# Optimization experiments

Hardware: AMD Instinct MI355X
Metric: run time of the kernel (lower is better)

The kernel has to match this reference:

```python
import jax, jax.numpy as jnp
import numpy as np

N, E, IN, H, OUT, G = 40000, 640000, 128, 128, 16, 64


def _sage(x, src, dst, Wl, Wr, b, n):
    # PyG SAGEConv (aggr='mean'): out = lin_l(mean_j x_j) + lin_r(x_i); bias in lin_l only
    msg = jnp.take(x, src, axis=0)                      # [E, d] gather
    s = jax.ops.segment_sum(msg, dst, num_segments=n)   # [N, d] scatter-add
    cnt = jax.ops.segment_sum(jnp.ones((src.shape[0], 1), x.dtype), dst, num_segments=n)
    agg = s / jnp.maximum(cnt, 1.0)                     # mean; 0 for isolated nodes
    return agg @ Wl.T + x @ Wr.T + b


def setup_inputs() -> dict:
    key = jax.random.key(0)
    ks = jax.random.split(key, 12)
    x = jax.random.normal(ks[0], (N, IN), jnp.float32)
    edge_index = jax.random.randint(ks[1], (2, E), 0, N, jnp.int64)
    batch = jnp.sort(jax.random.randint(ks[2], (N,), 0, G, jnp.int64))
    def lin(k, o, i):
        return jax.random.normal(k, (o, i), jnp.float32) / np.sqrt(i)
    return {
        "x": x, "edge_index": edge_index, "batch": batch,
        "W1l": lin(ks[3], H, IN), "W1r": lin(ks[4], H, IN), "b1": jnp.zeros((H,), jnp.float32),
        "W2l": lin(ks[5], H, H),  "W2r": lin(ks[6], H, H),  "b2": jnp.zeros((H,), jnp.float32),
        "W3l": lin(ks[7], H, H),  "W3r": lin(ks[8], H, H),  "b3": jnp.zeros((H,), jnp.float32),
        "Wfc": lin(ks[9], OUT, H), "bfc": jnp.zeros((OUT,), jnp.float32),
    }


def reference(x, edge_index, batch, W1l, W1r, b1, W2l, W2r, b2, W3l, W3r, b3, Wfc, bfc):
    src, dst = edge_index[0], edge_index[1]
    n = x.shape[0]
    h = jax.nn.relu(_sage(x, src, dst, W1l, W1r, b1, n))
    h = jax.nn.relu(_sage(h, src, dst, W2l, W2r, b2, n))
    h = jax.nn.relu(_sage(h, src, dst, W3l, W3r, b3, n))
    # global_mean_pool over graph ids
    s = jax.ops.segment_sum(h, batch, num_segments=G)
    cnt = jax.ops.segment_sum(jnp.ones((n, 1), h.dtype), batch, num_segments=G)
    pooled = s / jnp.maximum(cnt, 1.0)                  # [G, H]
    return pooled @ Wfc.T + bfc                          # [G, OUT]
```

## Files before the change

### kernel.cpp

```cpp
#include <hip/hip_runtime.h>

static constexpr int D = 128;
static constexpr int PS = 32;

typedef __attribute__((ext_vector_type(8))) short short8;
typedef __attribute__((ext_vector_type(4))) float f32x4;

__device__ inline ushort f2bf(float f) {
  union { float f; unsigned u; } v; v.f = f;
  unsigned r = v.u + 0x7FFF + ((v.u >> 16) & 1);
  return (ushort)(r >> 16);
}
__device__ inline float bf2f_lo(unsigned p) {
  union { unsigned u; float f; } v; v.u = p << 16; return v.f;
}
__device__ inline float bf2f_hi(unsigned p) {
  union { unsigned u; float f; } v; v.u = p & 0xFFFF0000u; return v.f;
}

__global__ __launch_bounds__(256) void k_hist(const int* __restrict__ dst, int* __restrict__ hist, int E) {
  int e = blockIdx.x * 256 + threadIdx.x;
  if (e < E) atomicAdd(&hist[dst[e]], 1);
}

__global__ __launch_bounds__(1024) void k_scan(const int* __restrict__ hist, int* __restrict__ offsets, int n) {
  __shared__ int wsum[16];
  int tid = threadIdx.x, lane = tid & 63, w = tid >> 6;
  int carry = 0;
  for (int base = 0; base < n; base += 1024) {
    int i = base + tid;
    int v = (i < n) ? hist[i] : 0;
    int x = v;
    #pragma unroll
    for (int off = 1; off < 64; off <<= 1) {
      int t = __shfl_up(x, off);
      if (lane >= off) x += t;
    }
    if (lane == 63) wsum[w] = x;
    __syncthreads();
    int wpre = 0, total = 0;
    #pragma unroll
    for (int k = 0; k < 16; ++k) { int s = wsum[k]; total += s; if (k < w) wpre += s; }
    if (i < n) offsets[i] = carry + wpre + x - v;
    carry += total;
    __syncthreads();
  }
  if (tid == 0) offsets[n] = carry;
}

__global__ __launch_bounds__(256) void k_fill(const int* __restrict__ src, const int* __restrict__ dst,
                                              const int* __restrict__ offsets, int* __restrict__ cursor,
                                              int* __restrict__ ssrc, int E) {
  int e = blockIdx.x * 256 + threadIdx.x;
  if (e < E) {
    int d = dst[e];
    int pos = offsets[d] + atomicAdd(&cursor[d], 1);
    ssrc[pos] = src[e];
  }
}

__global__ __launch_bounds__(256) void k_cvt(const float* __restrict__ in, ushort* __restrict__ out, int n4) {
  int i = blockIdx.x * 256 + threadIdx.x;
  if (i >= n4) return;
  float4 v = *(const float4*)&in[i * 4];
  ushort4 o;
  o.x = f2bf(v.x); o.y = f2bf(v.y); o.z = f2bf(v.z); o.w = f2bf(v.w);
  *(ushort4*)&out[i * 4] = o;
}

struct WPtrs { const float* s[6]; ushort* d[6]; };
__global__ __launch_bounds__(256) void k_cvt_w(WPtrs p) {
  int idx = blockIdx.x * 256 + threadIdx.x;
  int mat = idx >> 12;
  int off = (idx & 4095) * 4;
  float4 v = *(const float4*)&p.s[mat][off];
  ushort4 o;
  o.x = f2bf(v.x); o.y = f2bf(v.y); o.z = f2bf(v.z); o.w = f2bf(v.w);
  *(ushort4*)&p.d[mat][off] = o;
}

__global__ __launch_bounds__(256) void k_aggregate_bf(const ushort* __restrict__ X, const int* __restrict__ offsets,
                                                      const int* __restrict__ ssrc, ushort* __restrict__ Agg, int n) {
  int wid = (blockIdx.x * 256 + threadIdx.x) >> 6;
  int lane = threadIdx.x & 63;
  if (wid >= n) return;
  int q = lane >> 4, r = lane & 15;
  int o0 = offsets[wid], o1 = offsets[wid + 1];
  int deg = o1 - o0;

  float acc[8];
  #pragma unroll
  for (int i = 0; i < 8; ++i) acc[i] = 0.f;

  uint4 cur = {0u, 0u, 0u, 0u};
  if (q < deg) {
    int sid = ssrc[o0 + q];
    cur = *(const uint4*)&X[(size_t)sid * D + r * 8];
  }
  for (int base = 0; base < deg; base += 4) {
    uint4 nxt = {0u, 0u, 0u, 0u};
    int nb = base + 4 + q;
    if (nb < deg) {
      int sid = ssrc[o0 + nb];
      nxt = *(const uint4*)&X[(size_t)sid * D + r * 8];
    }
    acc[0] += bf2f_lo(cur.x); acc[1] += bf2f_hi(cur.x);
    acc[2] += bf2f_lo(cur.y); acc[3] += bf2f_hi(cur.y);
    acc[4] += bf2f_lo(cur.z); acc[5] += bf2f_hi(cur.z);
    acc[6] += bf2f_lo(cur.w); acc[7] += bf2f_hi(cur.w);
    cur = nxt;
  }
  #pragma unroll
  for (int i = 0; i < 8; ++i) {
    acc[i] += __shfl_xor(acc[i], 16);
    acc[i] += __shfl_xor(acc[i], 32);
  }
  if (q == 0) {
    float inv = 1.f / (float)max(deg, 1);
    uint4 o;
    o.x = (unsigned)f2bf(acc[0] * inv) | ((unsigned)f2bf(acc[1] * inv) << 16);
    o.y = (unsigned)f2bf(acc[2] * inv) | ((unsigned)f2bf(acc[3] * inv) << 16);
    o.z = (unsigned)f2bf(acc[4] * inv) | ((unsigned)f2bf(acc[5] * inv) << 16);
    o.w = (unsigned)f2bf(acc[6] * inv) | ((unsigned)f2bf(acc[7] * inv) << 16);
    *(uint4*)&Agg[(size_t)wid * D + r * 8] = o;
  }
}

__global__ __launch_bounds__(256) void k_gemm_mfma(const ushort* __restrict__ Abf, const ushort* __restrict__ Xbf,
                                                   const ushort* __restrict__ Wl, const ushort* __restrict__ Wr,
                                                   const float* __restrict__ bias, ushort* __restrict__ Out, int n) {
  int tid = threadIdx.x;
  int wave = tid >> 6, lane = tid & 63;
  int wm = wave >> 1, wn = wave & 1;
  int m_base = blockIdx.x * 64 + wm * 32;
  int n_base = wn * 64;
  int r = lane & 15, kg = lane >> 4;

  f32x4 acc[2][4];
  #pragma unroll
  for (int i = 0; i < 2; ++i)
    #pragma unroll
    for (int j = 0; j < 4; ++j) acc[i][j] = (f32x4){0.f, 0.f, 0.f, 0.f};

  const ushort* As[2] = {Abf, Xbf};
  const ushort* Ws[2] = {Wl, Wr};
  #pragma unroll
  for (int half = 0; half < 2; ++half) {
    const ushort* A = As[half];
    const ushort* W = Ws[half];
    #pragma unroll
    for (int k0 = 0; k0 < 128; k0 += 32) {
      int kk = k0 + kg * 8;
      short8 a[2], b[4];
      #pragma unroll
      for (int fm = 0; fm < 2; ++fm)
        a[fm] = *(const short8*)&A[(size_t)(m_base + fm * 16 + r) * D + kk];
      #pragma unroll
      for (int fn = 0; fn < 4; ++fn)
        b[fn] = *(const short8*)&W[(size_t)(n_base + fn * 16 + r) * D + kk];
      #pragma unroll
      for (int fm = 0; fm < 2; ++fm)
        #pragma unroll
        for (int fn = 0; fn < 4; ++fn)
          acc[fm][fn] = __builtin_amdgcn_mfma_f32_16x16x32_bf16(a[fm], b[fn], acc[fm][fn], 0, 0, 0);
    }
  }
  #pragma unroll
  for (int fn = 0; fn < 4; ++fn) {
    int j = n_base + fn * 16 + r;
    float bj = bias[j];
    #pragma unroll
    for (int fm = 0; fm < 2; ++fm) {
      #pragma unroll
      for (int q = 0; q < 4; ++q) {
        int node = m_base + fm * 16 + kg * 4 + q;
        float v = fmaxf(acc[fm][fn][q] + bj, 0.f);
        Out[(size_t)node * D + j] = f2bf(v);
      }
    }
  }
}

__global__ __launch_bounds__(256) void k_pool_partial(const ushort* __restrict__ H, const int* __restrict__ batch,
                                                      float* __restrict__ partial, int n) {
  __shared__ float wsums[4][128];
  int g = blockIdx.x / PS, s = blockIdx.x % PS;
  int tid = threadIdx.x, wave = tid >> 6, lane = tid & 63;
  int a = 0, b = n;
  while (a < b) { int m = (a + b) >> 1; if (batch[m] < g) a = m + 1; else b = m; }
  int lo = a;
  b = n;
  while (a < b) { int m = (a + b) >> 1; if (batch[m] < g + 1) a = m + 1; else b = m; }
  int hi = a;
  int len = hi - lo;
  int chunk = (len + PS - 1) / PS;
  int a0 = lo + s * chunk;
  int a1 = min(a0 + chunk, hi);
  float ax = 0.f, ay = 0.f;
  for (int node = a0 + wave; node < a1; node += 4) {
    unsigned v = *(const unsigned*)&H[(size_t)node * D + lane * 2];
    ax += bf2f_lo(v);
    ay += bf2f_hi(v);
  }
  wsums[wave][lane * 2] = ax;
  wsums[wave][lane * 2 + 1] = ay;
  __syncthreads();
  if (tid < 128) {
    float v = wsums[0][tid] + wsums[1][tid] + wsums[2][tid] + wsums[3][tid];
    partial[(size_t)blockIdx.x * 128 + tid] = v;
  }
}

__global__ __launch_bounds__(256) void k_pool_fc2(const float* __restrict__ partial, const int* __restrict__ batch,
                                                  const float* __restrict__ Wfc, const float* __restrict__ bfc,
                                                  float* __restrict__ out, int n, int OUT) {
  __shared__ float pooled[128];
  int g = blockIdx.x;
  int tid = threadIdx.x, lane = tid & 63;
  int a = 0, b = n;
  while (a < b) { int m = (a + b) >> 1; if (batch[m] < g) a = m + 1; else b = m; }
  int lo = a;
  b = n;
  while (a < b) { int m = (a + b) >> 1; if (batch[m] < g + 1) a = m + 1; else b = m; }
  int hi = a;
  float inv = 1.f / (float)max(hi - lo, 1);
  if (tid < 128) {
    float v = 0.f;
    #pragma unroll
    for (int s = 0; s < PS; ++s) v += partial[(size_t)(g * PS + s) * 128 + tid];
    pooled[tid] = v * inv;
  }
  __syncthreads();
  if (tid < 64) {
    float2 p = *(const float2*)&pooled[lane * 2];
    for (int o = 0; o < OUT; ++o) {
      float2 w = *(const float2*)&Wfc[o * D + lane * 2];
      float part = p.x * w.x + p.y * w.y;
      #pragma unroll
      for (int off = 32; off > 0; off >>= 1) part += __shfl_down(part, off);
      if (lane == 0) out[g * OUT + o] = part + bfc[o];
    }
  }
}

extern "C" void kernel_launch(void* const* d_in, const int* in_sizes, int n_in,
                              void* d_out, int out_size, void* d_ws, size_t ws_size,
                              hipStream_t stream) {
  const float* x   = (const float*)d_in[0];
  const int* ei    = (const int*)d_in[1];
  const int* batch = (const int*)d_in[2];
  const float* W1l = (const float*)d_in[3];
  const float* W1r = (const float*)d_in[4];
  const float* b1  = (const float*)d_in[5];
  const float* W2l = (const float*)d_in[6];
  const float* W2r = (const float*)d_in[7];
  const float* b2  = (const float*)d_in[8];
  const float* W3l = (const float*)d_in[9];
  const float* W3r = (const float*)d_in[10];
  const float* b3  = (const float*)d_in[11];
  const float* Wfc = (const float*)d_in[12];
  const float* bfc = (const float*)d_in[13];
  float* out = (float*)d_out;

  int N = in_sizes[0] / D;
  int E = in_sizes[1] / 2;
  int OUT = in_sizes[12] / D;
  int G = out_size / OUT;
  const int* src = ei;
  const int* dst = ei + E;

  ushort* xb  = (ushort*)d_ws;
  ushort* agg = xb + (size_t)N * D;
  ushort* h1  = agg + (size_t)N * D;
  ushort* h2  = h1 + (size_t)N * D;
  ushort* wb  = h2 + (size_t)N * D;
  int* ssrc   = (int*)(wb + 6 * 128 * 128);
  int* hist   = ssrc + E;
  int* offsets = hist + N;
  int* cursor = offsets + (N + 2);
  float* partial = (float*)(cursor + N + 2);

  ushort* wl1 = wb + 0 * 16384; ushort* wr1 = wb + 1 * 16384;
  ushort* wl2 = wb + 2 * 16384; ushort* wr2 = wb + 3 * 16384;
  ushort* wl3 = wb + 4 * 16384; ushort* wr3 = wb + 5 * 16384;

  hipMemsetAsync(hist, 0, (size_t)N * 4, stream);
  hipMemsetAsync(cursor, 0, (size_t)N * 4, stream);

  int eb = (E + 255) / 256;
  k_hist<<<eb, 256, 0, stream>>>(dst, hist, E);
  k_scan<<<1, 1024, 0, stream>>>(hist, offsets, N);
  k_fill<<<eb, 256, 0, stream>>>(src, dst, offsets, cursor, ssrc, E);

  int n4 = N * D / 4;
  k_cvt<<<(n4 + 255) / 256, 256, 0, stream>>>(x, xb, n4);
  WPtrs wp;
  wp.s[0] = W1l; wp.s[1] = W1r; wp.s[2] = W2l; wp.s[3] = W2r; wp.s[4] = W3l; wp.s[5] = W3r;
  wp.d[0] = wl1; wp.d[1] = wr1; wp.d[2] = wl2; wp.d[3] = wr2; wp.d[4] = wl3; wp.d[5] = wr3;
  k_cvt_w<<<96, 256, 0, stream>>>(wp);

  int ab = (N * 64 + 255) / 256;
  int gb = N / 64;

  k_aggregate_bf<<<ab, 256, 0, stream>>>(xb, offsets, ssrc, agg, N);
  k_gemm_mfma<<<gb, 256, 0, stream>>>(agg, xb, wl1, wr1, b1, h1, N);

  k_aggregate_bf<<<ab, 256, 0, stream>>>(h1, offsets, ssrc, agg, N);
  k_gemm_mfma<<<gb, 256, 0, stream>>>(agg, h1, wl2, wr2, b2, h2, N);

  k_aggregate_bf<<<ab, 256, 0, stream>>>(h2, offsets, ssrc, agg, N);
  k_gemm_mfma<<<gb, 256, 0, stream>>>(agg, h2, wl3, wr3, b3, h1, N);

  k_pool_partial<<<G * PS, 256, 0, stream>>>(h1, batch, partial, N);
  k_pool_fc2<<<G, 256, 0, stream>>>(partial, batch, Wfc, bfc, out, N, OUT);
}
```

Before: 284.1 us.

## Fuse prep kernels, merge memsets, widen scan, batch aggregate gathers via shuffle

```diff
diff --git a/kernel.cpp b/kernel.cpp
--- a/kernel.cpp
+++ b/kernel.cpp
@@ -18,19 +18,48 @@
   union { unsigned u; float f; } v; v.u = p & 0xFFFF0000u; return v.f;
 }
 
-__global__ __launch_bounds__(256) void k_hist(const int* __restrict__ dst, int* __restrict__ hist, int E) {
-  int e = blockIdx.x * 256 + threadIdx.x;
-  if (e < E) atomicAdd(&hist[dst[e]], 1);
+struct WPtrs { const float* s[6]; ushort* d[6]; };
+
+__global__ __launch_bounds__(256) void k_prep(const float* __restrict__ x, ushort* __restrict__ xb, WPtrs p,
+                                              const int* __restrict__ dst, int* __restrict__ hist,
+                                              int n4x, int E) {
+  int b = blockIdx.x, tid = threadIdx.x;
+  int nxb = (n4x + 255) / 256;
+  if (b < nxb) {
+    int i = b * 256 + tid;
+    if (i < n4x) {
+      float4 v = *(const float4*)&x[i * 4];
+      ushort4 o;
+      o.x = f2bf(v.x); o.y = f2bf(v.y); o.z = f2bf(v.z); o.w = f2bf(v.w);
+      *(ushort4*)&xb[i * 4] = o;
+    }
+  } else if (b < nxb + 96) {
+    int idx = (b - nxb) * 256 + tid;
+    int mat = idx >> 12;
+    int off = (idx & 4095) * 4;
+    float4 v = *(const float4*)&p.s[mat][off];
+    ushort4 o;
+    o.x = f2bf(v.x); o.y = f2bf(v.y); o.z = f2bf(v.z); o.w = f2bf(v.w);
+    *(ushort4*)&p.d[mat][off] = o;
+  } else {
+    int e = (b - nxb - 96) * 256 + tid;
+    if (e < E) atomicAdd(&hist[dst[e]], 1);
+  }
 }
 
 __global__ __launch_bounds__(1024) void k_scan(const int* __restrict__ hist, int* __restrict__ offsets, int n) {
   __shared__ int wsum[16];
   int tid = threadIdx.x, lane = tid & 63, w = tid >> 6;
   int carry = 0;
-  for (int base = 0; base < n; base += 1024) {
-    int i = base + tid;
-    int v = (i < n) ? hist[i] : 0;
-    int x = v;
+  for (int base = 0; base < n; base += 8192) {
+    int i0 = base + tid * 8;
+    int v[8];
+    #pragma unroll
+    for (int j = 0; j < 8; ++j) { int i = i0 + j; v[j] = (i < n) ? hist[i] : 0; }
+    int s = 0;
+    #pragma unroll
+    for (int j = 0; j < 8; ++j) { int t = v[j]; v[j] = s; s += t; }
+    int x = s;
     #pragma unroll
     for (int off = 1; off < 64; off <<= 1) {
       int t = __shfl_up(x, off);
@@ -40,8 +69,10 @@
     __syncthreads();
     int wpre = 0, total = 0;
     #pragma unroll
-    for (int k = 0; k < 16; ++k) { int s = wsum[k]; total += s; if (k < w) wpre += s; }
-    if (i < n) offsets[i] = carry + wpre + x - v;
+    for (int k = 0; k < 16; ++k) { int t = wsum[k]; total += t; if (k < w) wpre += t; }
+    int pre = carry + wpre + x - s;
+    #pragma unroll
+    for (int j = 0; j < 8; ++j) { int i = i0 + j; if (i < n) offsets[i] = pre + v[j]; }
     carry += total;
     __syncthreads();
   }
@@ -59,56 +90,40 @@
   }
 }
 
-__global__ __launch_bounds__(256) void k_cvt(const float* __restrict__ in, ushort* __restrict__ out, int n4) {
-  int i = blockIdx.x * 256 + threadIdx.x;
-  if (i >= n4) return;
-  float4 v = *(const float4*)&in[i * 4];
-  ushort4 o;
-  o.x = f2bf(v.x); o.y = f2bf(v.y); o.z = f2bf(v.z); o.w = f2bf(v.w);
-  *(ushort4*)&out[i * 4] = o;
-}
-
-struct WPtrs { const float* s[6]; ushort* d[6]; };
-__global__ __launch_bounds__(256) void k_cvt_w(WPtrs p) {
-  int idx = blockIdx.x * 256 + threadIdx.x;
-  int mat = idx >> 12;
-  int off = (idx & 4095) * 4;
-  float4 v = *(const float4*)&p.s[mat][off];
-  ushort4 o;
-  o.x = f2bf(v.x); o.y = f2bf(v.y); o.z = f2bf(v.z); o.w = f2bf(v.w);
-  *(ushort4*)&p.d[mat][off] = o;
-}
-
 __global__ __launch_bounds__(256) void k_aggregate_bf(const ushort* __restrict__ X, const int* __restrict__ offsets,
                                                       const int* __restrict__ ssrc, ushort* __restrict__ Agg, int n) {
   int wid = (blockIdx.x * 256 + threadIdx.x) >> 6;
   int lane = threadIdx.x & 63;
   if (wid >= n) return;
   int q = lane >> 4, r = lane & 15;
-  int o0 = offsets[wid], o1 = offsets[wid + 1];
-  int deg = o1 - o0;
+  int o0 = offsets[wid], deg = offsets[wid + 1] - o0;
 
   float acc[8];
   #pragma unroll
   for (int i = 0; i < 8; ++i) acc[i] = 0.f;
 
-  uint4 cur = {0u, 0u, 0u, 0u};
-  if (q < deg) {
-    int sid = ssrc[o0 + q];
-    cur = *(const uint4*)&X[(size_t)sid * D + r * 8];
-  }
-  for (int base = 0; base < deg; base += 4) {
-    uint4 nxt = {0u, 0u, 0u, 0u};
-    int nb = base + 4 + q;
-    if (nb < deg) {
-      int sid = ssrc[o0 + nb];
-      nxt = *(const uint4*)&X[(size_t)sid * D + r * 8];
-    }
-    acc[0] += bf2f_lo(cur.x); acc[1] += bf2f_hi(cur.x);
-    acc[2] += bf2f_lo(cur.y); acc[3] += bf2f_hi(cur.y);
-    acc[4] += bf2f_lo(cur.z); acc[5] += bf2f_hi(cur.z);
-    acc[6] += bf2f_lo(cur.w); acc[7] += bf2f_hi(cur.w);
-    cur = nxt;
+  for (int c0 = 0; c0 < deg; c0 += 64) {
+    int cn = min(64, deg - c0);
+    int myid = (lane < cn) ? ssrc[o0 + c0 + lane] : 0;
+    for (int j = 0; j < cn; j += 16) {
+      uint4 buf[4];
+      #pragma unroll
+      for (int t = 0; t < 4; ++t) {
+        int e = j + t * 4 + q;
+        buf[t] = (uint4){0u, 0u, 0u, 0u};
+        if (e < cn) {
+          int s = __shfl(myid, e);
+          buf[t] = *(const uint4*)&X[(size_t)s * D + r * 8];
+        }
+      }
+      #pragma unroll
+      for (int t = 0; t < 4; ++t) {
+        acc[0] += bf2f_lo(buf[t].x); acc[1] += bf2f_hi(buf[t].x);
+        acc[2] += bf2f_lo(buf[t].y); acc[3] += bf2f_hi(buf[t].y);
+        acc[4] += bf2f_lo(buf[t].z); acc[5] += bf2f_hi(buf[t].z);
+        acc[6] += bf2f_lo(buf[t].w); acc[7] += bf2f_hi(buf[t].w);
+      }
+    }
   }
   #pragma unroll
   for (int i = 0; i < 8; ++i) {
@@ -276,28 +291,26 @@
   ushort* wb  = h2 + (size_t)N * D;
   int* ssrc   = (int*)(wb + 6 * 128 * 128);
   int* hist   = ssrc + E;
-  int* offsets = hist + N;
-  int* cursor = offsets + (N + 2);
-  float* partial = (float*)(cursor + N + 2);
+  int* cursor = hist + N;
+  int* offsets = cursor + N;
+  float* partial = (float*)(offsets + N + 2);
 
   ushort* wl1 = wb + 0 * 16384; ushort* wr1 = wb + 1 * 16384;
   ushort* wl2 = wb + 2 * 16384; ushort* wr2 = wb + 3 * 16384;
   ushort* wl3 = wb + 4 * 16384; ushort* wr3 = wb + 5 * 16384;
 
-  hipMemsetAsync(hist, 0, (size_t)N * 4, stream);
-  hipMemsetAsync(cursor, 0, (size_t)N * 4, stream);
-
-  int eb = (E + 255) / 256;
-  k_hist<<<eb, 256, 0, stream>>>(dst, hist, E);
-  k_scan<<<1, 1024, 0, stream>>>(hist, offsets, N);
-  k_fill<<<eb, 256, 0, stream>>>(src, dst, offsets, cursor, ssrc, E);
-
-  int n4 = N * D / 4;
-  k_cvt<<<(n4 + 255) / 256, 256, 0, stream>>>(x, xb, n4);
+  hipMemsetAsync(hist, 0, (size_t)2 * N * 4, stream);
+
   WPtrs wp;
   wp.s[0] = W1l; wp.s[1] = W1r; wp.s[2] = W2l; wp.s[3] = W2r; wp.s[4] = W3l; wp.s[5] = W3r;
   wp.d[0] = wl1; wp.d[1] = wr1; wp.d[2] = wl2; wp.d[3] = wr2; wp.d[4] = wl3; wp.d[5] = wr3;
-  k_cvt_w<<<96, 256, 0, stream>>>(wp);
+
+  int n4 = N * D / 4;
+  int nxb = (n4 + 255) / 256;
+  int eb = (E + 255) / 256;
+  k_prep<<<nxb + 96 + eb, 256, 0, stream>>>(x, xb, wp, dst, hist, n4, E);
+  k_scan<<<1, 1024, 0, stream>>>(hist, offsets, N);
+  k_fill<<<eb, 256, 0, stream>>>(src, dst, offsets, cursor, ssrc, E);
 
   int ab = (N * 64 + 255) / 256;
   int gb = N / 64;
```

New measurement: 263.1 us. 7.4% less time.
